# Performance work log

Hardware: AMD Instinct MI355X
Metric: run time of the kernel (lower is better)

The kernel has to match this reference:

```python
import jax, jax.numpy as jnp
import numpy as np

B, T, D, NH, L, E, K = 2, 1024, 512, 8, 4, 8, 2
H = D * 4
HD = D // NH
EPS = 1e-5
THETA = 10000.0
MOE_LAYERS = (0, 2)   # layer_idx % moe_freq == 0
DENSE_LAYERS = (1, 3)


def setup_inputs() -> dict:
    key = jax.random.key(0)
    ks = jax.random.split(key, 12)
    s = 0.02
    return {
        "x": jax.random.normal(ks[0], (B, T, D), jnp.float32),
        "qkv_w": jax.random.normal(ks[1], (L, 3 * D, D), jnp.float32) * s,
        "out_w": jax.random.normal(ks[2], (L, D, D), jnp.float32) * s,
        "norm1_w": jnp.ones((L, D), jnp.float32),
        "norm2_w": jnp.ones((L, D), jnp.float32),
        "router_w": jax.random.normal(ks[3], (2, E, D), jnp.float32) * s,
        "moe_w1": jax.random.normal(ks[4], (2, E, H, D), jnp.float32) * s,
        "moe_w2": jax.random.normal(ks[5], (2, E, D, H), jnp.float32) * s,
        "moe_w3": jax.random.normal(ks[6], (2, E, H, D), jnp.float32) * s,
        "f_w1": jax.random.normal(ks[7], (2, H, D), jnp.float32) * s,
        "f_w2": jax.random.normal(ks[8], (2, D, H), jnp.float32) * s,
        "f_w3": jax.random.normal(ks[9], (2, H, D), jnp.float32) * s,
        "norm_f": jnp.ones((D,), jnp.float32),
    }


def rmsnorm(x, w):
    return w * x * jax.lax.rsqrt(jnp.mean(x * x, axis=-1, keepdims=True) + EPS)


def rope_tables():
    inv_freq = 1.0 / (THETA ** (jnp.arange(0, HD, 2, dtype=jnp.float32) / HD))  # [HD/2]
    t = jnp.arange(T, dtype=jnp.float32)
    freqs = t[:, None] * inv_freq[None, :]  # [T, HD/2]
    return jnp.cos(freqs), jnp.sin(freqs)


def apply_rope(x, cos, sin):  # x: [B, NH, T, HD]
    x1, x2 = jnp.split(x, 2, axis=-1)
    return jnp.concatenate([x1 * cos - x2 * sin, x1 * sin + x2 * cos], axis=-1)


def attention(x, qkv_w, out_w, cos, sin, causal):
    qkv = x @ qkv_w.T  # [B, T, 3D]
    q, k, v = jnp.split(qkv, 3, axis=-1)
    sh = lambda a: a.reshape(B, T, NH, HD).transpose(0, 2, 1, 3)  # [B, NH, T, HD]
    q, k, v = sh(q), sh(k), sh(v)
    q = apply_rope(q, cos, sin)
    k = apply_rope(k, cos, sin)
    scores = jnp.einsum('bhqd,bhkd->bhqk', q, k) / np.sqrt(HD).astype(np.float32)
    scores = jnp.where(causal, scores, jnp.finfo(scores.dtype).min)
    attn = jax.nn.softmax(scores, axis=-1)
    out = jnp.einsum('bhqk,bhkd->bhqd', attn, v)
    out = out.transpose(0, 2, 1, 3).reshape(B, T, D)
    return out @ out_w.T


def swiglu(x, w1, w2, w3):
    return (jax.nn.silu(x @ w1.T) * (x @ w3.T)) @ w2.T


def moe(x, rw, w1, w2, w3):  # x: [N, D]
    n = x.shape[0]
    logits = x @ rw.T                              # [N, E]
    top_v, top_i = jax.lax.top_k(logits, K)        # [N, K]
    wts = jax.nn.softmax(top_v, axis=-1)           # [N, K]
    # combine[t, e] = sum_i wts[t, i] * 1[top_i[t, i] == e]
    combine = jnp.zeros((n, E), x.dtype).at[jnp.arange(n)[:, None], top_i].add(wts)
    gate = jax.nn.silu(jnp.einsum('nd,ehd->neh', x, w1))
    up = jnp.einsum('nd,ehd->neh', x, w3)
    expert_out = jnp.einsum('neh,edh->ned', gate * up, w2)  # [N, E, D]
    return jnp.einsum('ne,ned->nd', combine, expert_out)


def reference(x, qkv_w, out_w, norm1_w, norm2_w, router_w, moe_w1, moe_w2,
              moe_w3, f_w1, f_w2, f_w3, norm_f):
    cos, sin = rope_tables()
    causal = jnp.tril(jnp.ones((T, T), bool))
    h = x
    for l in range(L):
        h = h + attention(rmsnorm(h, norm1_w[l]), qkv_w[l], out_w[l], cos, sin, causal)
        hn = rmsnorm(h, norm2_w[l])
        if l in MOE_LAYERS:
            m = MOE_LAYERS.index(l)
            ff = moe(hn.reshape(-1, D), router_w[m], moe_w1[m], moe_w2[m], moe_w3[m]).reshape(B, T, D)
        else:
            m = DENSE_LAYERS.index(l)
            ff = swiglu(hn, f_w1[m], f_w2[m], f_w3[m])
        h = h + ff
    return rmsnorm(h, norm_f)
```

## Files before the change

kernel.cpp:

```cpp
#include <hip/hip_runtime.h>
#include <hip/hip_bf16.h>
#include <math.h>

#define Bc 2
#define Tc 1024
#define Dc 512
#define NHc 8
#define Lc 4
#define Ec 8
#define Kc 2
#define Hc 2048
#define HDc 64
#define Nc (Bc * Tc)
#define NKc (Nc * Kc)

typedef __bf16 bf16x8 __attribute__((ext_vector_type(8)));
typedef float  f32x4  __attribute__((ext_vector_type(4)));
typedef unsigned short ushort8v __attribute__((ext_vector_type(8)));
typedef unsigned short ushort4v __attribute__((ext_vector_type(4)));

__device__ inline unsigned short f2bf(float f) {
    union { float f; unsigned u; } v; v.f = f;
    unsigned r = v.u + 0x7FFFu + ((v.u >> 16) & 1u);
    return (unsigned short)(r >> 16);
}
__device__ inline float bf2f(unsigned short b) {
    union { unsigned u; float f; } v; v.u = ((unsigned)b) << 16;
    return v.f;
}
__device__ inline void splitbf(float a, unsigned short& hi, unsigned short& lo) {
    unsigned short h = f2bf(a);
    hi = h;
    lo = f2bf(a - bf2f(h));
}
__device__ inline void split8(const float4& a, const float4& b,
                              ushort8v& h, ushort8v& l) {
    unsigned short hh, ll;
    splitbf(a.x, hh, ll); h[0] = hh; l[0] = ll;
    splitbf(a.y, hh, ll); h[1] = hh; l[1] = ll;
    splitbf(a.z, hh, ll); h[2] = hh; l[2] = ll;
    splitbf(a.w, hh, ll); h[3] = hh; l[3] = ll;
    splitbf(b.x, hh, ll); h[4] = hh; l[4] = ll;
    splitbf(b.y, hh, ll); h[5] = hh; l[5] = ll;
    splitbf(b.z, hh, ll); h[6] = hh; l[6] = ll;
    splitbf(b.w, hh, ll); h[7] = hh; l[7] = ll;
}

__global__ __launch_bounds__(256) void split_w_kernel(
    const float* __restrict__ w, unsigned short* __restrict__ hi,
    unsigned short* __restrict__ lo, int n4)
{
    int i = blockIdx.x * 256 + threadIdx.x;
    if (i >= n4) return;
    float4 v = ((const float4*)w)[i];
    ushort4v h, l;
    unsigned short a, b;
    splitbf(v.x, a, b); h[0] = a; l[0] = b;
    splitbf(v.y, a, b); h[1] = a; l[1] = b;
    splitbf(v.z, a, b); h[2] = a; l[2] = b;
    splitbf(v.w, a, b); h[3] = a; l[3] = b;
    ((ushort4v*)hi)[i] = h;
    ((ushort4v*)lo)[i] = l;
}

__global__ __launch_bounds__(256) void rmsnorm_split_kernel(
    const float* __restrict__ x, const float* __restrict__ w,
    float* __restrict__ y, unsigned short* __restrict__ yh,
    unsigned short* __restrict__ yl)
{
    int row = blockIdx.x;
    const float* xr = x + (size_t)row * Dc;
    __shared__ float red[256];
    int tid = threadIdx.x;
    float ss = 0.0f;
    for (int d = tid; d < Dc; d += 256) { float v = xr[d]; ss += v * v; }
    red[tid] = ss; __syncthreads();
    for (int s = 128; s > 0; s >>= 1) {
        if (tid < s) red[tid] += red[tid + s];
        __syncthreads();
    }
    float inv = rsqrtf(red[0] / (float)Dc + 1e-5f);
    for (int d = tid; d < Dc; d += 256) {
        float v = w[d] * xr[d] * inv;
        size_t idx = (size_t)row * Dc + d;
        y[idx] = v;
        unsigned short h, l;
        splitbf(v, h, l);
        yh[idx] = h; yl[idx] = l;
    }
}

__global__ __launch_bounds__(256) void rmsnorm_kernel(
    const float* __restrict__ x, const float* __restrict__ w,
    float* __restrict__ y)
{
    int row = blockIdx.x;
    const float* xr = x + (size_t)row * Dc;
    __shared__ float red[256];
    int tid = threadIdx.x;
    float ss = 0.0f;
    for (int d = tid; d < Dc; d += 256) { float v = xr[d]; ss += v * v; }
    red[tid] = ss; __syncthreads();
    for (int s = 128; s > 0; s >>= 1) {
        if (tid < s) red[tid] += red[tid + s];
        __syncthreads();
    }
    float inv = rsqrtf(red[0] / (float)Dc + 1e-5f);
    for (int d = tid; d < Dc; d += 256)
        y[(size_t)row * Dc + d] = w[d] * xr[d] * inv;
}

template<int MODE, int TM, int TN>
__global__ __launch_bounds__(256) void gemm3p(
    const unsigned short* __restrict__ Ahi, const unsigned short* __restrict__ Alo,
    const unsigned short* __restrict__ Whibase, const unsigned short* __restrict__ Wlobase,
    float* __restrict__ C, int M, int N, int K,
    const int* __restrict__ tok, const float* __restrict__ twt,
    const int* __restrict__ counts, const int* __restrict__ offsets,
    size_t wstride)
{
    constexpr int PAD = 40;
    constexpr int PA  = TM / 64;
    constexpr int PB  = TN / 64;
    constexpr int FM  = TM / 32;
    constexpr int FN  = TN / 32;

    int e = (MODE == 5) ? blockIdx.z : 0;
    int count = M, offs = 0;
    if (MODE == 5) {
        count = counts[e];
        offs  = offsets[e];
        if ((int)(blockIdx.y * TM) >= count) return;
    }
    const unsigned short* Whi = Whibase + (size_t)e * wstride;
    const unsigned short* Wlo = Wlobase + (size_t)e * wstride;

    __shared__ __align__(16) unsigned short Ah[TM][PAD];
    __shared__ __align__(16) unsigned short Al[TM][PAD];
    __shared__ __align__(16) unsigned short Bh[TN][PAD];
    __shared__ __align__(16) unsigned short Bl[TN][PAD];

    int tid = threadIdx.x;
    int m0 = blockIdx.y * TM, n0 = blockIdx.x * TN;
    int srow = tid >> 2;
    int scol = (tid & 3) * 8;

    int wave = tid >> 6, lane = tid & 63;
    int wm = wave >> 1, wn = wave & 1;
    int quad = lane >> 4, l16 = lane & 15;

    f32x4 acc[FM][FN];
#pragma unroll
    for (int mi = 0; mi < FM; ++mi)
#pragma unroll
        for (int ni = 0; ni < FN; ++ni)
            acc[mi][ni] = (f32x4){0.f, 0.f, 0.f, 0.f};

    size_t arow[PA];
#pragma unroll
    for (int p = 0; p < PA; ++p) {
        int row = p * 64 + srow;
        if (MODE == 5) {
            int rr = m0 + row; if (rr >= count) rr = 0;
            arow[p] = (size_t)(offs + rr) * K;
        } else {
            arow[p] = (size_t)(m0 + row) * K;
        }
    }
    size_t brow[PB];
#pragma unroll
    for (int p = 0; p < PB; ++p)
        brow[p] = (size_t)(n0 + p * 64 + srow) * K;

    ushort8v pah[PA], pal[PA], pbh[PB], pbl[PB];
#pragma unroll
    for (int p = 0; p < PA; ++p) {
        pah[p] = *(const ushort8v*)(Ahi + arow[p] + scol);
        pal[p] = *(const ushort8v*)(Alo + arow[p] + scol);
    }
#pragma unroll
    for (int p = 0; p < PB; ++p) {
        pbh[p] = *(const ushort8v*)(Whi + brow[p] + scol);
        pbl[p] = *(const ushort8v*)(Wlo + brow[p] + scol);
    }

    for (int k0 = 0; k0 < K; k0 += 32) {
#pragma unroll
        for (int p = 0; p < PA; ++p) {
            int row = p * 64 + srow;
            *(ushort8v*)&Ah[row][scol] = pah[p];
            *(ushort8v*)&Al[row][scol] = pal[p];
        }
#pragma unroll
        for (int p = 0; p < PB; ++p) {
            int row = p * 64 + srow;
            *(ushort8v*)&Bh[row][scol] = pbh[p];
            *(ushort8v*)&Bl[row][scol] = pbl[p];
        }
        __syncthreads();
        if (k0 + 32 < K) {
            int kn = k0 + 32;
#pragma unroll
            for (int p = 0; p < PA; ++p) {
                pah[p] = *(const ushort8v*)(Ahi + arow[p] + kn + scol);
                pal[p] = *(const ushort8v*)(Alo + arow[p] + kn + scol);
            }
#pragma unroll
            for (int p = 0; p < PB; ++p) {
                pbh[p] = *(const ushort8v*)(Whi + brow[p] + kn + scol);
                pbl[p] = *(const ushort8v*)(Wlo + brow[p] + kn + scol);
            }
        }

        bf16x8 ah[FM], al[FM], bh[FN], bl[FN];
#pragma unroll
        for (int mi = 0; mi < FM; ++mi) {
            ah[mi] = *(const bf16x8*)&Ah[wm * (TM / 2) + mi * 16 + l16][quad * 8];
            al[mi] = *(const bf16x8*)&Al[wm * (TM / 2) + mi * 16 + l16][quad * 8];
        }
#pragma unroll
        for (int ni = 0; ni < FN; ++ni) {
            bh[ni] = *(const bf16x8*)&Bh[wn * (TN / 2) + ni * 16 + l16][quad * 8];
            bl[ni] = *(const bf16x8*)&Bl[wn * (TN / 2) + ni * 16 + l16][quad * 8];
        }
#pragma unroll
        for (int mi = 0; mi < FM; ++mi)
#pragma unroll
            for (int ni = 0; ni < FN; ++ni) {
                acc[mi][ni] = __builtin_amdgcn_mfma_f32_16x16x32_bf16(
                    ah[mi], bh[ni], acc[mi][ni], 0, 0, 0);
                acc[mi][ni] = __builtin_amdgcn_mfma_f32_16x16x32_bf16(
                    al[mi], bh[ni], acc[mi][ni], 0, 0, 0);
                acc[mi][ni] = __builtin_amdgcn_mfma_f32_16x16x32_bf16(
                    ah[mi], bl[ni], acc[mi][ni], 0, 0, 0);
            }
        __syncthreads();
    }

#pragma unroll
    for (int mi = 0; mi < FM; ++mi) {
#pragma unroll
        for (int ni = 0; ni < FN; ++ni) {
            int col = n0 + wn * (TN / 2) + ni * 16 + l16;
#pragma unroll
            for (int r = 0; r < 4; ++r) {
                int row = wm * (TM / 2) + mi * 16 + quad * 4 + r;
                float v = acc[mi][ni][r];
                if (MODE == 0) {
                    C[(size_t)(m0 + row) * N + col] = v;
                } else if (MODE == 1) {
                    C[(size_t)(m0 + row) * N + col] += v;
                } else {
                    int rr = m0 + row;
                    if (rr < count) {
                        int dest = tok[offs + rr];
                        float w = twt[offs + rr];
                        atomicAdd(&C[(size_t)dest * N + col], w * v);
                    }
                }
            }
        }
    }
}

template<bool GATHER>
__global__ __launch_bounds__(256) void ffn_fusedp(
    const unsigned short* __restrict__ Ahi, const unsigned short* __restrict__ Alo,
    const unsigned short* __restrict__ W1hibase, const unsigned short* __restrict__ W1lobase,
    const unsigned short* __restrict__ W3hibase, const unsigned short* __restrict__ W3lobase,
    unsigned short* __restrict__ Thi, unsigned short* __restrict__ Tlo,
    int M, int N, int K,
    const int* __restrict__ tok, const int* __restrict__ counts,
    const int* __restrict__ offsets, size_t wstride)
{
    constexpr int TM = 64, TN = 128, PAD = 40;
    constexpr int FM = 2, FN = 4;

    int e = GATHER ? blockIdx.z : 0;
    int count = M, offs = 0;
    if (GATHER) {
        count = counts[e];
        offs  = offsets[e];
        if ((int)(blockIdx.y * TM) >= count) return;
    }
    const unsigned short* W1hi = W1hibase + (size_t)e * wstride;
    const unsigned short* W1lo = W1lobase + (size_t)e * wstride;
    const unsigned short* W3hi = W3hibase + (size_t)e * wstride;
    const unsigned short* W3lo = W3lobase + (size_t)e * wstride;

    __shared__ __align__(16) unsigned short Ah[TM][PAD];
    __shared__ __align__(16) unsigned short Al[TM][PAD];
    __shared__ __align__(16) unsigned short B1h[TN][PAD];
    __shared__ __align__(16) unsigned short B1l[TN][PAD];
    __shared__ __align__(16) unsigned short B3h[TN][PAD];
    __shared__ __align__(16) unsigned short B3l[TN][PAD];
    __shared__ int sTok[TM];

    int tid = threadIdx.x;
    int m0 = blockIdx.y * TM, n0 = blockIdx.x * TN;

    if (GATHER) {
        if (tid < TM) {
            int r = m0 + tid;
            sTok[tid] = (r < count) ? tok[offs + r] : tok[offs];
        }
        __syncthreads();
    }

    int srow = tid >> 2;
    int scol = (tid & 3) * 8;
    int wave = tid >> 6, lane = tid & 63;
    int wm = wave >> 1, wn = wave & 1;
    int quad = lane >> 4, l16 = lane & 15;

    f32x4 accg[FM][FN], accu[FM][FN];
#pragma unroll
    for (int mi = 0; mi < FM; ++mi)
#pragma unroll
        for (int ni = 0; ni < FN; ++ni) {
            accg[mi][ni] = (f32x4){0.f, 0.f, 0.f, 0.f};
            accu[mi][ni] = (f32x4){0.f, 0.f, 0.f, 0.f};
        }

    size_t arow;
    if (GATHER) arow = (size_t)sTok[srow] * K;
    else        arow = (size_t)(m0 + srow) * K;
    size_t brow[2];
    brow[0] = (size_t)(n0 + srow) * K;
    brow[1] = (size_t)(n0 + 64 + srow) * K;

    ushort8v pah, pal, p1h[2], p1l[2], p3h[2], p3l[2];
    pah = *(const ushort8v*)(Ahi + arow + scol);
    pal = *(const ushort8v*)(Alo + arow + scol);
#pragma unroll
    for (int p = 0; p < 2; ++p) {
        p1h[p] = *(const ushort8v*)(W1hi + brow[p] + scol);
        p1l[p] = *(const ushort8v*)(W1lo + brow[p] + scol);
        p3h[p] = *(const ushort8v*)(W3hi + brow[p] + scol);
        p3l[p] = *(const ushort8v*)(W3lo + brow[p] + scol);
    }

    for (int k0 = 0; k0 < K; k0 += 32) {
        *(ushort8v*)&Ah[srow][scol] = pah;
        *(ushort8v*)&Al[srow][scol] = pal;
#pragma unroll
        for (int p = 0; p < 2; ++p) {
            int row = p * 64 + srow;
            *(ushort8v*)&B1h[row][scol] = p1h[p];
            *(ushort8v*)&B1l[row][scol] = p1l[p];
            *(ushort8v*)&B3h[row][scol] = p3h[p];
            *(ushort8v*)&B3l[row][scol] = p3l[p];
        }
        __syncthreads();
        if (k0 + 32 < K) {
            int kn = k0 + 32;
            pah = *(const ushort8v*)(Ahi + arow + kn + scol);
            pal = *(const ushort8v*)(Alo + arow + kn + scol);
#pragma unroll
            for (int p = 0; p < 2; ++p) {
                p1h[p] = *(const ushort8v*)(W1hi + brow[p] + kn + scol);
                p1l[p] = *(const ushort8v*)(W1lo + brow[p] + kn + scol);
                p3h[p] = *(const ushort8v*)(W3hi + brow[p] + kn + scol);
                p3l[p] = *(const ushort8v*)(W3lo + brow[p] + kn + scol);
            }
        }

        bf16x8 ah[FM], al[FM], bh[FN], bl[FN];
#pragma unroll
        for (int mi = 0; mi < FM; ++mi) {
            ah[mi] = *(const bf16x8*)&Ah[wm * 32 + mi * 16 + l16][quad * 8];
            al[mi] = *(const bf16x8*)&Al[wm * 32 + mi * 16 + l16][quad * 8];
        }
#pragma unroll
        for (int ni = 0; ni < FN; ++ni) {
            bh[ni] = *(const bf16x8*)&B1h[wn * 64 + ni * 16 + l16][quad * 8];
            bl[ni] = *(const bf16x8*)&B1l[wn * 64 + ni * 16 + l16][quad * 8];
        }
#pragma unroll
        for (int mi = 0; mi < FM; ++mi)
#pragma unroll
            for (int ni = 0; ni < FN; ++ni) {
                accg[mi][ni] = __builtin_amdgcn_mfma_f32_16x16x32_bf16(
                    ah[mi], bh[ni], accg[mi][ni], 0, 0, 0);
                accg[mi][ni] = __builtin_amdgcn_mfma_f32_16x16x32_bf16(
                    al[mi], bh[ni], accg[mi][ni], 0, 0, 0);
                accg[mi][ni] = __builtin_amdgcn_mfma_f32_16x16x32_bf16(
                    ah[mi], bl[ni], accg[mi][ni], 0, 0, 0);
            }
#pragma unroll
        for (int ni = 0; ni < FN; ++ni) {
            bh[ni] = *(const bf16x8*)&B3h[wn * 64 + ni * 16 + l16][quad * 8];
            bl[ni] = *(const bf16x8*)&B3l[wn * 64 + ni * 16 + l16][quad * 8];
        }
#pragma unroll
        for (int mi = 0; mi < FM; ++mi)
#pragma unroll
            for (int ni = 0; ni < FN; ++ni) {
                accu[mi][ni] = __builtin_amdgcn_mfma_f32_16x16x32_bf16(
                    ah[mi], bh[ni], accu[mi][ni], 0, 0, 0);
                accu[mi][ni] = __builtin_amdgcn_mfma_f32_16x16x32_bf16(
                    al[mi], bh[ni], accu[mi][ni], 0, 0, 0);
                accu[mi][ni] = __builtin_amdgcn_mfma_f32_16x16x32_bf16(
                    ah[mi], bl[ni], accu[mi][ni], 0, 0, 0);
            }
        __syncthreads();
    }

#pragma unroll
    for (int mi = 0; mi < FM; ++mi) {
#pragma unroll
        for (int ni = 0; ni < FN; ++ni) {
            int col = n0 + wn * 64 + ni * 16 + l16;
#pragma unroll
            for (int r = 0; r < 4; ++r) {
                int row = wm * 32 + mi * 16 + quad * 4 + r;
                float g = accg[mi][ni][r];
                float u = accu[mi][ni][r];
                float t = (g / (1.0f + expf(-g))) * u;
                unsigned short th, tl;
                splitbf(t, th, tl);
                if (GATHER) {
                    int rr = m0 + row;
                    if (rr < count) {
                        size_t idx = (size_t)(offs + rr) * N + col;
                        Thi[idx] = th; Tlo[idx] = tl;
                    }
                } else {
                    size_t idx = (size_t)(m0 + row) * N + col;
                    Thi[idx] = th; Tlo[idx] = tl;
                }
            }
        }
    }
}

__global__ __launch_bounds__(256) void rope_kernel(float* __restrict__ qkv)
{
    const int HD2 = HDc / 2;
    int idx = blockIdx.x * blockDim.x + threadIdx.x;
    int total = Nc * NHc * HD2;
    if (idx >= total) return;
    int i = idx % HD2;
    int hh = (idx / HD2) % NHc;
    int n = idx / (HD2 * NHc);
    int t = n % Tc;
    float invf = expf(-(2.0f * (float)i / (float)HDc) * logf(10000.0f));
    float f = (float)t * invf;
    float c = cosf(f), s = sinf(f);
    size_t base = (size_t)n * (3 * Dc) + (size_t)hh * HDc;
    float* qp = qkv + base;
    float* kp = qkv + base + Dc;
    float q1 = qp[i], q2 = qp[i + HD2];
    qp[i]       = q1 * c - q2 * s;
    qp[i + HD2] = q1 * s + q2 * c;
    float k1 = kp[i], k2 = kp[i + HD2];
    kp[i]       = k1 * c - k2 * s;
    kp[i + HD2] = k1 * s + k2 * c;
}

__global__ __launch_bounds__(256) void attn_mfma(
    const float* __restrict__ qkv, unsigned short* __restrict__ outh,
    unsigned short* __restrict__ outl)
{
    constexpr int PAD = 72;
    __shared__ __align__(16) unsigned short Qh[64][PAD];
    __shared__ __align__(16) unsigned short Ql[64][PAD];
    __shared__ __align__(16) unsigned short Kh[64][PAD];
    __shared__ __align__(16) unsigned short Kl[64][PAD];
    __shared__ __align__(16) unsigned short Vth[64][PAD];
    __shared__ __align__(16) unsigned short Vtl[64][PAD];

    int qb = blockIdx.x, bh = blockIdx.y;
    int b = bh >> 3, hh = bh & 7;
    const int D3 = 3 * Dc;
    const float* base = qkv + (size_t)b * Tc * D3 + (size_t)hh * HDc;

    int tid = threadIdx.x;
    int wave = tid >> 6, lane = tid & 63;
    int quad = lane >> 4, l16 = lane & 15;

    int srow = tid >> 2;
    int scb  = (tid & 3) * 16;
    int vhd  = lane;
    int vkb  = wave * 16;

    {
        const float* qp = base + (size_t)(qb * 64 + srow) * D3 + scb;
        float4 q0 = *(const float4*)(qp);
        float4 q1 = *(const float4*)(qp + 4);
        float4 q2 = *(const float4*)(qp + 8);
        float4 q3 = *(const float4*)(qp + 12);
        const float sc = 0.125f;
        q0.x *= sc; q0.y *= sc; q0.z *= sc; q0.w *= sc;
        q1.x *= sc; q1.y *= sc; q1.z *= sc; q1.w *= sc;
        q2.x *= sc; q2.y *= sc; q2.z *= sc; q2.w *= sc;
        q3.x *= sc; q3.y *= sc; q3.z *= sc; q3.w *= sc;
        ushort8v h, l;
        split8(q0, q1, h, l);
        *(ushort8v*)&Qh[srow][scb]     = h;
        *(ushort8v*)&Ql[srow][scb]     = l;
        split8(q2, q3, h, l);
        *(ushort8v*)&Qh[srow][scb + 8] = h;
        *(ushort8v*)&Ql[srow][scb + 8] = l;
    }
    __syncthreads();
    bf16x8 qah[2], qal[2];
#pragma unroll
    for (int ks = 0; ks < 2; ++ks) {
        qah[ks] = *(const bf16x8*)&Qh[wave * 16 + l16][ks * 32 + quad * 8];
        qal[ks] = *(const bf16x8*)&Ql[wave * 16 + l16][ks * 32 + quad * 8];
    }

    float4 kf0, kf1, kf2, kf3;
    float vf[16];
    {
        const float* kp = base + (size_t)srow * D3 + Dc + scb;
        kf0 = *(const float4*)(kp);
        kf1 = *(const float4*)(kp + 4);
        kf2 = *(const float4*)(kp + 8);
        kf3 = *(const float4*)(kp + 12);
        const float* vp = base + (size_t)vkb * D3 + 2 * Dc + vhd;
#pragma unroll
        for (int i = 0; i < 16; ++i) vf[i] = vp[(size_t)i * D3];
    }

    f32x4 o[4];
#pragma unroll
    for (int f = 0; f < 4; ++f) o[f] = (f32x4){0.f, 0.f, 0.f, 0.f};
    float mrow[4], lrow[4];
#pragma unroll
    for (int r = 0; r < 4; ++r) { mrow[r] = -1e30f; lrow[r] = 0.0f; }

    for (int kt = 0; kt <= qb; ++kt) {
        __syncthreads();
        {
            ushort8v h, l;
            split8(kf0, kf1, h, l);
            *(ushort8v*)&Kh[srow][scb]     = h;
            *(ushort8v*)&Kl[srow][scb]     = l;
            split8(kf2, kf3, h, l);
            *(ushort8v*)&Kh[srow][scb + 8] = h;
            *(ushort8v*)&Kl[srow][scb + 8] = l;
        }
        {
            float4 v0 = make_float4(vf[0], vf[1], vf[2], vf[3]);
            float4 v1 = make_float4(vf[4], vf[5], vf[6], vf[7]);
            float4 v2 = make_float4(vf[8], vf[9], vf[10], vf[11]);
            float4 v3 = make_float4(vf[12], vf[13], vf[14], vf[15]);
            ushort8v h, l;
            split8(v0, v1, h, l);
            *(ushort8v*)&Vth[vhd][vkb]     = h;
            *(ushort8v*)&Vtl[vhd][vkb]     = l;
            split8(v2, v3, h, l);
            *(ushort8v*)&Vth[vhd][vkb + 8] = h;
            *(ushort8v*)&Vtl[vhd][vkb + 8] = l;
        }
        __syncthreads();
        if (kt < qb) {
            const float* kp = base + (size_t)((kt + 1) * 64 + srow) * D3 + Dc + scb;
            kf0 = *(const float4*)(kp);
            kf1 = *(const float4*)(kp + 4);
            kf2 = *(const float4*)(kp + 8);
            kf3 = *(const float4*)(kp + 12);
            const float* vp = base + (size_t)((kt + 1) * 64 + vkb) * D3 + 2 * Dc + vhd;
#pragma unroll
            for (int i = 0; i < 16; ++i) vf[i] = vp[(size_t)i * D3];
        }

        f32x4 s[4];
#pragma unroll
        for (int ni = 0; ni < 4; ++ni) s[ni] = (f32x4){0.f, 0.f, 0.f, 0.f};
#pragma unroll
        for (int ks = 0; ks < 2; ++ks) {
            bf16x8 kh_[4], kl_[4];
#pragma unroll
            for (int ni = 0; ni < 4; ++ni) {
                kh_[ni] = *(const bf16x8*)&Kh[ni * 16 + l16][ks * 32 + quad * 8];
                kl_[ni] = *(const bf16x8*)&Kl[ni * 16 + l16][ks * 32 + quad * 8];
            }
#pragma unroll
            for (int ni = 0; ni < 4; ++ni) {
                s[ni] = __builtin_amdgcn_mfma_f32_16x16x32_bf16(
                    qah[ks], kh_[ni], s[ni], 0, 0, 0);
                s[ni] = __builtin_amdgcn_mfma_f32_16x16x32_bf16(
                    qal[ks], kh_[ni], s[ni], 0, 0, 0);
                s[ni] = __builtin_amdgcn_mfma_f32_16x16x32_bf16(
                    qah[ks], kl_[ni], s[ni], 0, 0, 0);
            }
        }

        if (kt == qb) {
#pragma unroll
            for (int ni = 0; ni < 4; ++ni)
#pragma unroll
                for (int r = 0; r < 4; ++r)
                    if (ni * 16 + l16 > wave * 16 + quad * 4 + r)
                        s[ni][r] = -1e30f;
        }

        float al4[4];
#pragma unroll
        for (int r = 0; r < 4; ++r) {
            float rm = fmaxf(fmaxf(s[0][r], s[1][r]), fmaxf(s[2][r], s[3][r]));
            rm = fmaxf(rm, __shfl_xor(rm, 1));
            rm = fmaxf(rm, __shfl_xor(rm, 2));
            rm = fmaxf(rm, __shfl_xor(rm, 4));
            rm = fmaxf(rm, __shfl_xor(rm, 8));
            float mn = fmaxf(mrow[r], rm);
            al4[r] = __expf(mrow[r] - mn);
            mrow[r] = mn;
            float rs = 0.0f;
#pragma unroll
            for (int ni = 0; ni < 4; ++ni) {
                float pv = __expf(s[ni][r] - mn);
                s[ni][r] = pv;
                rs += pv;
            }
            rs += __shfl_xor(rs, 1);
            rs += __shfl_xor(rs, 2);
            rs += __shfl_xor(rs, 4);
            rs += __shfl_xor(rs, 8);
            lrow[r] = lrow[r] * al4[r] + rs;
        }

        __syncthreads();
#pragma unroll
        for (int ni = 0; ni < 4; ++ni)
#pragma unroll
            for (int r = 0; r < 4; ++r) {
                unsigned short hp, lp;
                splitbf(s[ni][r], hp, lp);
                Kh[wave * 16 + quad * 4 + r][ni * 16 + l16] = hp;
                Kl[wave * 16 + quad * 4 + r][ni * 16 + l16] = lp;
            }
#pragma unroll
        for (int f = 0; f < 4; ++f)
#pragma unroll
            for (int r = 0; r < 4; ++r)
                o[f][r] *= al4[r];
#pragma unroll
        for (int ks = 0; ks < 2; ++ks) {
            bf16x8 pah = *(const bf16x8*)&Kh[wave * 16 + l16][ks * 32 + quad * 8];
            bf16x8 pal = *(const bf16x8*)&Kl[wave * 16 + l16][ks * 32 + quad * 8];
#pragma unroll
            for (int f = 0; f < 4; ++f) {
                bf16x8 vh_ = *(const bf16x8*)&Vth[f * 16 + l16][ks * 32 + quad * 8];
                bf16x8 vl_ = *(const bf16x8*)&Vtl[f * 16 + l16][ks * 32 + quad * 8];
                o[f] = __builtin_amdgcn_mfma_f32_16x16x32_bf16(
                    pah, vh_, o[f], 0, 0, 0);
                o[f] = __builtin_amdgcn_mfma_f32_16x16x32_bf16(
                    pal, vh_, o[f], 0, 0, 0);
                o[f] = __builtin_amdgcn_mfma_f32_16x16x32_bf16(
                    pah, vl_, o[f], 0, 0, 0);
            }
        }
    }

#pragma unroll
    for (int r = 0; r < 4; ++r) {
        float inv = 1.0f / lrow[r];
        int q = qb * 64 + wave * 16 + quad * 4 + r;
#pragma unroll
        for (int f = 0; f < 4; ++f) {
            size_t idx = (size_t)(b * Tc + q) * Dc + hh * HDc + f * 16 + l16;
            unsigned short hp, lp;
            splitbf(o[f][r] * inv, hp, lp);
            outh[idx] = hp; outl[idx] = lp;
        }
    }
}

__global__ __launch_bounds__(64) void router_kernel(
    const float* __restrict__ x, const float* __restrict__ rw,
    float* __restrict__ logits)
{
    int n = blockIdx.x;
    int lane = threadIdx.x;
    const float* xr = x + (size_t)n * Dc;
    for (int e = 0; e < Ec; ++e) {
        const float* wr = rw + (size_t)e * Dc;
        float p = 0.0f;
        for (int d = lane; d < Dc; d += 64) p += xr[d] * wr[d];
        for (int off = 32; off > 0; off >>= 1) p += __shfl_down(p, off);
        if (lane == 0) logits[(size_t)n * Ec + e] = p;
    }
}

__global__ void zero8_kernel(int* __restrict__ counts)
{
    if (threadIdx.x < Ec) counts[threadIdx.x] = 0;
}

__global__ __launch_bounds__(256) void topk_count_kernel(
    const float* __restrict__ logits, int* __restrict__ counts,
    int2* __restrict__ eidx, float2* __restrict__ ewt)
{
    int n = blockIdx.x * blockDim.x + threadIdx.x;
    if (n >= Nc) return;
    const float* lg = logits + (size_t)n * Ec;
    int i0 = -1, i1 = -1;
    float v0 = -1e30f, v1 = -1e30f;
    for (int e = 0; e < Ec; ++e) {
        float v = lg[e];
        if (v > v0) { v1 = v0; i1 = i0; v0 = v; i0 = e; }
        else if (v > v1) { v1 = v; i1 = e; }
    }
    float e1 = expf(v1 - v0);
    float w0 = 1.0f / (1.0f + e1);
    float w1 = e1 / (1.0f + e1);
    atomicAdd(&counts[i0], 1);
    atomicAdd(&counts[i1], 1);
    eidx[n] = make_int2(i0, i1);
    ewt[n]  = make_float2(w0, w1);
}

__global__ void scan_kernel(int* __restrict__ counts, int* __restrict__ offsets)
{
    if (threadIdx.x == 0) {
        int s = 0;
        for (int e = 0; e < Ec; ++e) { offsets[e] = s; s += counts[e]; counts[e] = 0; }
    }
}

__global__ __launch_bounds__(256) void topk_place_kernel(
    const int2* __restrict__ eidx, const float2* __restrict__ ewt,
    int* __restrict__ counts, const int* __restrict__ offsets,
    int* __restrict__ tok, float* __restrict__ twt)
{
    int n = blockIdx.x * blockDim.x + threadIdx.x;
    if (n >= Nc) return;
    int2 ei = eidx[n];
    float2 w = ewt[n];
    int p0 = atomicAdd(&counts[ei.x], 1);
    int r0 = offsets[ei.x] + p0;
    tok[r0] = n; twt[r0] = w.x;
    int p1 = atomicAdd(&counts[ei.y], 1);
    int r1 = offsets[ei.y] + p1;
    tok[r1] = n; twt[r1] = w.y;
}

extern "C" void kernel_launch(void* const* d_in, const int* in_sizes, int n_in,
                              void* d_out, int out_size, void* d_ws, size_t ws_size,
                              hipStream_t stream)
{
    const float* x        = (const float*)d_in[0];
    const float* qkv_w    = (const float*)d_in[1];
    const float* out_w    = (const float*)d_in[2];
    const float* norm1_w  = (const float*)d_in[3];
    const float* norm2_w  = (const float*)d_in[4];
    const float* router_w = (const float*)d_in[5];
    const float* moe_w1   = (const float*)d_in[6];
    const float* moe_w2   = (const float*)d_in[7];
    const float* moe_w3   = (const float*)d_in[8];
    const float* f_w1     = (const float*)d_in[9];
    const float* f_w2     = (const float*)d_in[10];
    const float* f_w3     = (const float*)d_in[11];
    const float* norm_f   = (const float*)d_in[12];
    float* out = (float*)d_out;

    float* p = (float*)d_ws;
    float* h      = p;  p += Nc * Dc;
    float* xn     = p;  p += Nc * Dc;
    unsigned short* xnh = (unsigned short*)p;  p += Nc * Dc / 2;
    unsigned short* xnl = (unsigned short*)p;  p += Nc * Dc / 2;
    float* arena  = p;  p += (size_t)NKc * Hc;
    float* logits = p;  p += Nc * Ec;
    int*   counts  = (int*)p;  p += 16;
    int*   offsets = (int*)p;  p += 16;
    int2*  eidx    = (int2*)p; p += 2 * Nc;
    float* ewt     = p;        p += 2 * Nc;
    int*   tok     = (int*)p;  p += NKc;
    float* twt     = p;        p += NKc;
    unsigned short* wqh = (unsigned short*)p;
    unsigned short* wql = wqh + (size_t)3 * Dc * Dc;
    unsigned short* woh = wql + (size_t)3 * Dc * Dc;
    unsigned short* wol = woh + (size_t)Dc * Dc;
    unsigned short* wah = wol + (size_t)Dc * Dc;
    unsigned short* wal = wah + (size_t)Ec * Hc * Dc;
    unsigned short* wbh = wal + (size_t)Ec * Hc * Dc;
    unsigned short* wbl = wbh + (size_t)Ec * Hc * Dc;

    float* qkv = arena;
    unsigned short* th = (unsigned short*)arena;
    unsigned short* tl = th + (size_t)NKc * Hc;

    hipMemcpyAsync(h, x, (size_t)Nc * Dc * sizeof(float),
                   hipMemcpyDeviceToDevice, stream);

    for (int l = 0; l < Lc; ++l) {
        {
            int n4 = 3 * Dc * Dc / 4;
            split_w_kernel<<<(n4 + 255) / 256, 256, 0, stream>>>(
                qkv_w + (size_t)l * 3 * Dc * Dc, wqh, wql, n4);
        }
        rmsnorm_split_kernel<<<Nc, 256, 0, stream>>>(
            h, norm1_w + (size_t)l * Dc, xn, xnh, xnl);
        gemm3p<0, 64, 128><<<dim3(3 * Dc / 128, Nc / 64, 1), 256, 0, stream>>>(
            xnh, xnl, wqh, wql, qkv, Nc, 3 * Dc, Dc,
            nullptr, nullptr, nullptr, nullptr, 0);
        {
            int total = Nc * NHc * (HDc / 2);
            rope_kernel<<<(total + 255) / 256, 256, 0, stream>>>(qkv);
        }
        {
            int n4 = Dc * Dc / 4;
            split_w_kernel<<<(n4 + 255) / 256, 256, 0, stream>>>(
                out_w + (size_t)l * Dc * Dc, woh, wol, n4);
        }
        attn_mfma<<<dim3(Tc / 64, Bc * NHc), 256, 0, stream>>>(qkv, xnh, xnl);
        gemm3p<1, 64, 64><<<dim3(Dc / 64, Nc / 64, 1), 256, 0, stream>>>(
            xnh, xnl, woh, wol, h, Nc, Dc, Dc,
            nullptr, nullptr, nullptr, nullptr, 0);

        rmsnorm_split_kernel<<<Nc, 256, 0, stream>>>(
            h, norm2_w + (size_t)l * Dc, xn, xnh, xnl);
        if (l == 0 || l == 2) {
            int m = l / 2;
            router_kernel<<<Nc, 64, 0, stream>>>(
                xn, router_w + (size_t)m * Ec * Dc, logits);
            zero8_kernel<<<1, 64, 0, stream>>>(counts);
            topk_count_kernel<<<Nc / 256, 256, 0, stream>>>(
                logits, counts, eidx, (float2*)ewt);
            scan_kernel<<<1, 64, 0, stream>>>(counts, offsets);
            topk_place_kernel<<<Nc / 256, 256, 0, stream>>>(
                eidx, (float2*)ewt, counts, offsets, tok, twt);

            int n4 = Ec * Hc * Dc / 4;
            split_w_kernel<<<(n4 + 255) / 256, 256, 0, stream>>>(
                moe_w1 + (size_t)m * Ec * Hc * Dc, wah, wal, n4);
            split_w_kernel<<<(n4 + 255) / 256, 256, 0, stream>>>(
                moe_w3 + (size_t)m * Ec * Hc * Dc, wbh, wbl, n4);
            ffn_fusedp<true><<<dim3(Hc / 128, NKc / 64, Ec), 256, 0, stream>>>(
                xnh, xnl, wah, wal, wbh, wbl, th, tl, Nc, Hc, Dc,
                tok, counts, offsets, (size_t)Hc * Dc);
            split_w_kernel<<<(n4 + 255) / 256, 256, 0, stream>>>(
                moe_w2 + (size_t)m * Ec * Dc * Hc, wah, wal, n4);
            gemm3p<5, 64, 64><<<dim3(Dc / 64, NKc / 64, Ec), 256, 0, stream>>>(
                th, tl, wah, wal, h, Nc, Dc, Hc,
                tok, twt, counts, offsets, (size_t)Dc * Hc);
        } else {
            int m = (l - 1) / 2;
            int n4 = Hc * Dc / 4;
            split_w_kernel<<<(n4 + 255) / 256, 256, 0, stream>>>(
                f_w1 + (size_t)m * Hc * Dc, wah, wal, n4);
            split_w_kernel<<<(n4 + 255) / 256, 256, 0, stream>>>(
                f_w3 + (size_t)m * Hc * Dc, wbh, wbl, n4);
            ffn_fusedp<false><<<dim3(Hc / 128, Nc / 64, 1), 256, 0, stream>>>(
                xnh, xnl, wah, wal, wbh, wbl, th, tl, Nc, Hc, Dc,
                nullptr, nullptr, nullptr, 0);
            split_w_kernel<<<(n4 + 255) / 256, 256, 0, stream>>>(
                f_w2 + (size_t)m * Dc * Hc, wah, wal, n4);
            gemm3p<1, 64, 64><<<dim3(Dc / 64, Nc / 64, 1), 256, 0, stream>>>(
                th, tl, wah, wal, h, Nc, Dc, Hc,
                nullptr, nullptr, nullptr, nullptr, 0);
        }
    }

    rmsnorm_kernel<<<Nc, 256, 0, stream>>>(h, norm_f, out);
}
```

Before: 1.382 ms.

## Double-buffer GEMM prefetch, add XCD-aware block swizzle, widen down-proj tile

The gemm3p main loop now keeps two register prefetch buffers, so global loads run two K-steps ahead of the MFMA work. Both gemm3p and ffn_fusedp remap block indices with an XCD swizzle so that neighbouring tiles land on the same XCD and share its L2. The down-projection GEMM launches switch to 64x128 tiles. The extra buffers raise register pressure and may lower occupancy. The MoE early-exit test now uses the remapped row index, and the swizzle is applied per expert slice of z.

```diff
diff --git a/kernel.cpp b/kernel.cpp
--- a/kernel.cpp
+++ b/kernel.cpp
@@ -46,6 +46,12 @@
     splitbf(b.w, hh, ll); h[7] = hh; l[7] = ll;
 }
 
+__device__ inline int xcd_swizzle(int orig, int nwg) {
+    int q = nwg >> 3, r = nwg & 7;
+    int xcd = orig & 7, slot = orig >> 3;
+    return (xcd < r ? xcd * (q + 1) : r * (q + 1) + (xcd - r) * q) + slot;
+}
+
 __global__ __launch_bounds__(256) void split_w_kernel(
     const float* __restrict__ w, unsigned short* __restrict__ hi,
     unsigned short* __restrict__ lo, int n4)
@@ -130,10 +136,14 @@
     if (MODE == 5) {
         count = counts[e];
         offs  = offsets[e];
-        if ((int)(blockIdx.y * TM) >= count) return;
     }
     const unsigned short* Whi = Whibase + (size_t)e * wstride;
     const unsigned short* Wlo = Wlobase + (size_t)e * wstride;
+
+    int nwg  = gridDim.x * gridDim.y;
+    int wgid = xcd_swizzle(blockIdx.y * gridDim.x + blockIdx.x, nwg);
+    int bx = wgid % gridDim.x, by = wgid / gridDim.x;
+    if (MODE == 5 && by * TM >= count) return;
 
     __shared__ __align__(16) unsigned short Ah[TM][PAD];
     __shared__ __align__(16) unsigned short Al[TM][PAD];
@@ -141,7 +151,7 @@
     __shared__ __align__(16) unsigned short Bl[TN][PAD];
 
     int tid = threadIdx.x;
-    int m0 = blockIdx.y * TM, n0 = blockIdx.x * TN;
+    int m0 = by * TM, n0 = bx * TN;
     int srow = tid >> 2;
     int scol = (tid & 3) * 8;
 
@@ -172,70 +182,80 @@
     for (int p = 0; p < PB; ++p)
         brow[p] = (size_t)(n0 + p * 64 + srow) * K;
 
-    ushort8v pah[PA], pal[PA], pbh[PB], pbl[PB];
-#pragma unroll
-    for (int p = 0; p < PA; ++p) {
-        pah[p] = *(const ushort8v*)(Ahi + arow[p] + scol);
-        pal[p] = *(const ushort8v*)(Alo + arow[p] + scol);
-    }
-#pragma unroll
-    for (int p = 0; p < PB; ++p) {
-        pbh[p] = *(const ushort8v*)(Whi + brow[p] + scol);
-        pbl[p] = *(const ushort8v*)(Wlo + brow[p] + scol);
-    }
-
-    for (int k0 = 0; k0 < K; k0 += 32) {
-#pragma unroll
-        for (int p = 0; p < PA; ++p) {
-            int row = p * 64 + srow;
-            *(ushort8v*)&Ah[row][scol] = pah[p];
-            *(ushort8v*)&Al[row][scol] = pal[p];
-        }
-#pragma unroll
-        for (int p = 0; p < PB; ++p) {
-            int row = p * 64 + srow;
-            *(ushort8v*)&Bh[row][scol] = pbh[p];
-            *(ushort8v*)&Bl[row][scol] = pbl[p];
-        }
-        __syncthreads();
-        if (k0 + 32 < K) {
-            int kn = k0 + 32;
-#pragma unroll
-            for (int p = 0; p < PA; ++p) {
-                pah[p] = *(const ushort8v*)(Ahi + arow[p] + kn + scol);
-                pal[p] = *(const ushort8v*)(Alo + arow[p] + kn + scol);
-            }
-#pragma unroll
-            for (int p = 0; p < PB; ++p) {
-                pbh[p] = *(const ushort8v*)(Whi + brow[p] + kn + scol);
-                pbl[p] = *(const ushort8v*)(Wlo + brow[p] + kn + scol);
-            }
-        }
-
-        bf16x8 ah[FM], al[FM], bh[FN], bl[FN];
-#pragma unroll
-        for (int mi = 0; mi < FM; ++mi) {
-            ah[mi] = *(const bf16x8*)&Ah[wm * (TM / 2) + mi * 16 + l16][quad * 8];
-            al[mi] = *(const bf16x8*)&Al[wm * (TM / 2) + mi * 16 + l16][quad * 8];
-        }
-#pragma unroll
-        for (int ni = 0; ni < FN; ++ni) {
-            bh[ni] = *(const bf16x8*)&Bh[wn * (TN / 2) + ni * 16 + l16][quad * 8];
-            bl[ni] = *(const bf16x8*)&Bl[wn * (TN / 2) + ni * 16 + l16][quad * 8];
-        }
-#pragma unroll
-        for (int mi = 0; mi < FM; ++mi)
-#pragma unroll
-            for (int ni = 0; ni < FN; ++ni) {
-                acc[mi][ni] = __builtin_amdgcn_mfma_f32_16x16x32_bf16(
-                    ah[mi], bh[ni], acc[mi][ni], 0, 0, 0);
-                acc[mi][ni] = __builtin_amdgcn_mfma_f32_16x16x32_bf16(
-                    al[mi], bh[ni], acc[mi][ni], 0, 0, 0);
-                acc[mi][ni] = __builtin_amdgcn_mfma_f32_16x16x32_bf16(
-                    ah[mi], bl[ni], acc[mi][ni], 0, 0, 0);
-            }
-        __syncthreads();
-    }
+#define G3_LOAD(AH, AL, BH, BL, KN)                                       \
+    {                                                                     \
+        _Pragma("unroll")                                                 \
+        for (int p = 0; p < PA; ++p) {                                    \
+            AH[p] = *(const ushort8v*)(Ahi + arow[p] + (KN) + scol);      \
+            AL[p] = *(const ushort8v*)(Alo + arow[p] + (KN) + scol);      \
+        }                                                                 \
+        _Pragma("unroll")                                                 \
+        for (int p = 0; p < PB; ++p) {                                    \
+            BH[p] = *(const ushort8v*)(Whi + brow[p] + (KN) + scol);      \
+            BL[p] = *(const ushort8v*)(Wlo + brow[p] + (KN) + scol);      \
+        }                                                                 \
+    }
+
+#define G3_STORE(AH, AL, BH, BL)                                          \
+    {                                                                     \
+        _Pragma("unroll")                                                 \
+        for (int p = 0; p < PA; ++p) {                                    \
+            *(ushort8v*)&Ah[p * 64 + srow][scol] = AH[p];                 \
+            *(ushort8v*)&Al[p * 64 + srow][scol] = AL[p];                 \
+        }                                                                 \
+        _Pragma("unroll")                                                 \
+        for (int p = 0; p < PB; ++p) {                                    \
+            *(ushort8v*)&Bh[p * 64 + srow][scol] = BH[p];                 \
+            *(ushort8v*)&Bl[p * 64 + srow][scol] = BL[p];                 \
+        }                                                                 \
+    }
+
+#define G3_COMPUTE()                                                      \
+    {                                                                     \
+        bf16x8 ah[FM], al[FM], bh[FN], bl[FN];                            \
+        _Pragma("unroll")                                                 \
+        for (int mi = 0; mi < FM; ++mi) {                                 \
+            ah[mi] = *(const bf16x8*)&Ah[wm * (TM / 2) + mi * 16 + l16][quad * 8]; \
+            al[mi] = *(const bf16x8*)&Al[wm * (TM / 2) + mi * 16 + l16][quad * 8]; \
+        }                                                                 \
+        _Pragma("unroll")                                                 \
+        for (int ni = 0; ni < FN; ++ni) {                                 \
+            bh[ni] = *(const bf16x8*)&Bh[wn * (TN / 2) + ni * 16 + l16][quad * 8]; \
+            bl[ni] = *(const bf16x8*)&Bl[wn * (TN / 2) + ni * 16 + l16][quad * 8]; \
+        }                                                                 \
+        _Pragma("unroll")                                                 \
+        for (int mi = 0; mi < FM; ++mi)                                   \
+            _Pragma("unroll")                                             \
+            for (int ni = 0; ni < FN; ++ni) {                             \
+                acc[mi][ni] = __builtin_amdgcn_mfma_f32_16x16x32_bf16(    \
+                    ah[mi], bh[ni], acc[mi][ni], 0, 0, 0);                \
+                acc[mi][ni] = __builtin_amdgcn_mfma_f32_16x16x32_bf16(    \
+                    al[mi], bh[ni], acc[mi][ni], 0, 0, 0);                \
+                acc[mi][ni] = __builtin_amdgcn_mfma_f32_16x16x32_bf16(    \
+                    ah[mi], bl[ni], acc[mi][ni], 0, 0, 0);                \
+            }                                                             \
+    }
+
+    ushort8v a0h[PA], a0l[PA], b0h[PB], b0l[PB];
+    ushort8v a1h[PA], a1l[PA], b1h[PB], b1l[PB];
+    G3_LOAD(a0h, a0l, b0h, b0l, 0)
+    G3_LOAD(a1h, a1l, b1h, b1l, 32)
+
+    for (int k0 = 0; k0 < K; k0 += 64) {
+        G3_STORE(a0h, a0l, b0h, b0l)
+        __syncthreads();
+        if (k0 + 64 < K) G3_LOAD(a0h, a0l, b0h, b0l, k0 + 64)
+        G3_COMPUTE()
+        __syncthreads();
+        G3_STORE(a1h, a1l, b1h, b1l)
+        __syncthreads();
+        if (k0 + 96 < K) G3_LOAD(a1h, a1l, b1h, b1l, k0 + 96)
+        G3_COMPUTE()
+        __syncthreads();
+    }
+#undef G3_LOAD
+#undef G3_STORE
+#undef G3_COMPUTE
 
 #pragma unroll
     for (int mi = 0; mi < FM; ++mi) {
@@ -281,12 +301,16 @@
     if (GATHER) {
         count = counts[e];
         offs  = offsets[e];
-        if ((int)(blockIdx.y * TM) >= count) return;
     }
     const unsigned short* W1hi = W1hibase + (size_t)e * wstride;
     const unsigned short* W1lo = W1lobase + (size_t)e * wstride;
     const unsigned short* W3hi = W3hibase + (size_t)e * wstride;
     const unsigned short* W3lo = W3lobase + (size_t)e * wstride;
+
+    int nwg  = gridDim.x * gridDim.y;
+    int wgid = xcd_swizzle(blockIdx.y * gridDim.x + blockIdx.x, nwg);
+    int bx = wgid % gridDim.x, by = wgid / gridDim.x;
+    if (GATHER && by * TM >= count) return;
 
     __shared__ __align__(16) unsigned short Ah[TM][PAD];
     __shared__ __align__(16) unsigned short Al[TM][PAD];
@@ -297,7 +321,7 @@
     __shared__ int sTok[TM];
 
     int tid = threadIdx.x;
-    int m0 = blockIdx.y * TM, n0 = blockIdx.x * TN;
+    int m0 = by * TM, n0 = bx * TN;
 
     if (GATHER) {
         if (tid < TM) {
@@ -835,7 +859,7 @@
                 tok, counts, offsets, (size_t)Hc * Dc);
             split_w_kernel<<<(n4 + 255) / 256, 256, 0, stream>>>(
                 moe_w2 + (size_t)m * Ec * Dc * Hc, wah, wal, n4);
-            gemm3p<5, 64, 64><<<dim3(Dc / 64, NKc / 64, Ec), 256, 0, stream>>>(
+            gemm3p<5, 64, 128><<<dim3(Dc / 128, NKc / 64, Ec), 256, 0, stream>>>(
                 th, tl, wah, wal, h, Nc, Dc, Hc,
                 tok, twt, counts, offsets, (size_t)Dc * Hc);
         } else {
@@ -850,7 +874,7 @@
                 nullptr, nullptr, nullptr, 0);
             split_w_kernel<<<(n4 + 255) / 256, 256, 0, stream>>>(
                 f_w2 + (size_t)m * Dc * Hc, wah, wal, n4);
-            gemm3p<1, 64, 64><<<dim3(Dc / 64, Nc / 64, 1), 256, 0, stream>>>(
+            gemm3p<1, 64, 128><<<dim3(Dc / 128, Nc / 64, 1), 256, 0, stream>>>(
                 th, tl, wah, wal, h, Nc, Dc, Hc,
                 nullptr, nullptr, nullptr, nullptr, 0);
         }
```

Result: slower. 2.512 ms (+81.8%).
